# Kernel tuning notes

Hardware: AMD Instinct MI355X
Metric: run time of the kernel (lower is better)

Reference implementation:

```python
import jax, jax.numpy as jnp
import numpy as np
import math

NUM_HEADS = 12


def setup_inputs() -> dict:
    key = jax.random.key(0)
    ks = jax.random.split(key, 8)
    B, H, W, C = 8, 32, 32, 768
    dh = C // NUM_HEADS
    s = 0.02
    return {
        "x": jax.random.normal(ks[0], (B, H, W, C), dtype=jnp.float32),
        "w_qkv": jax.random.normal(ks[1], (C, 3 * C), dtype=jnp.float32) * s,
        "b_qkv": jnp.zeros((3 * C,), dtype=jnp.float32),
        "w_out": jax.random.normal(ks[2], (C, C), dtype=jnp.float32) * s,
        "b_out": jnp.zeros((C,), dtype=jnp.float32),
        "rel_pos_h": jax.random.normal(ks[3], (2 * H - 1, dh), dtype=jnp.float32) * s,
        "rel_pos_w": jax.random.normal(ks[4], (2 * W - 1, dh), dtype=jnp.float32) * s,
    }


def reference(x, w_qkv, b_qkv, w_out, b_out, rel_pos_h, rel_pos_w):
    B, H, W, C = x.shape
    nh = NUM_HEADS
    dh = C // nh
    scale = math.sqrt(dh)

    # QKV projection: (B, H*W, 3C) -> (3, B*nh, H*W, dh)
    qkv = jnp.einsum("bhwc,cf->bhwf", x, w_qkv) + b_qkv
    qkv = qkv.reshape(B, H * W, 3, nh, dh).transpose(2, 0, 3, 1, 4)
    qkv = qkv.reshape(3, B * nh, H * W, dh)
    q, k, v = qkv[0], qkv[1], qkv[2]

    scores = jnp.einsum("bqd,bkd->bqk", q, k) / scale  # (B*nh, HW, HW)

    # Decomposed relative position bias (q_size == k_size == input_size,
    # so get_rel_pos is a pure gather, no interpolation).
    coords_h = jnp.arange(H)[:, None] - jnp.arange(H)[None, :] + (H - 1)
    coords_w = jnp.arange(W)[:, None] - jnp.arange(W)[None, :] + (W - 1)
    Rh = rel_pos_h[coords_h]  # (H, H, dh)
    Rw = rel_pos_w[coords_w]  # (W, W, dh)
    r_q = q.reshape(B * nh, H, W, dh)
    rel_h = jnp.einsum("bhwc,hkc->bhwk", r_q, Rh)  # (B*nh, H, W, H)
    rel_w = jnp.einsum("bhwc,wkc->bhwk", r_q, Rw)  # (B*nh, H, W, W)
    scores = (
        scores.reshape(B * nh, H, W, H, W)
        + rel_h[:, :, :, :, None]
        + rel_w[:, :, :, None, :]
    ).reshape(B * nh, H * W, H * W)

    weights = jax.nn.softmax(scores, axis=-1)
    out = jnp.einsum("bqk,bkd->bqd", weights, v)  # (B*nh, HW, dh)
    out = out.reshape(B, nh, H, W, dh).transpose(0, 2, 3, 1, 4).reshape(B, H, W, C)
    return jnp.einsum("bhwc,cf->bhwf", out, w_out) + b_out
```

## Files before the change

### kernel.cpp

```cpp
#include <hip/hip_runtime.h>
#include <stdint.h>

#define NH 12
#define DH 64
#define HW_ 32
#define SEQ 1024
#define CDIM 768
#define BATCH 8
#define BHN (BATCH*NH)

#define LOG2E 1.44269504f
#define KSCALE 0.18033688f

typedef unsigned short u16;
typedef __attribute__((ext_vector_type(4))) float f32x4;
typedef __attribute__((ext_vector_type(8))) short bf16x8;

static __device__ __forceinline__ u16 f2bf(float f) {
  union { float f; unsigned u; } v; v.f = f;
  unsigned r = v.u + 0x7fff + ((v.u >> 16) & 1);
  return (u16)(r >> 16);
}
static __device__ __forceinline__ float bf2f(u16 h) {
  union { unsigned u; float f; } v; v.u = ((unsigned)h) << 16;
  return v.f;
}
static __device__ __forceinline__ unsigned pk_bf2(float a, float b) {
  union { float f; unsigned u; } ua, ub; ua.f = a; ub.f = b;
  return __builtin_amdgcn_perm(ub.u + 0x8000u, ua.u + 0x8000u, 0x07060302u);
}

#define GLDS(gp, lp) __builtin_amdgcn_global_load_lds( \
  (const __attribute__((address_space(1))) unsigned int*)(gp), \
  (__attribute__((address_space(3))) unsigned int*)(lp), 16, 0, 0)

__device__ __forceinline__ void transcvt_body(const float* __restrict__ w, u16* __restrict__ wt,
                                              int R, int C, int bx, int by, int tid) {
  __shared__ float t[64][65];
  const int tx = tid & 63, ty = tid >> 6;
  int c0 = bx * 64, r0 = by * 64;
  #pragma unroll
  for (int i = 0; i < 16; ++i) {
    int r = ty + i * 4;
    t[r][tx] = w[(size_t)(r0 + r) * C + c0 + tx];
  }
  __syncthreads();
  #pragma unroll
  for (int i = 0; i < 16; ++i) {
    int c = ty + i * 4;
    wt[(size_t)(c0 + c) * R + r0 + tx] = f2bf(t[tx][c]);
  }
}

__global__ void k_prep(const float* __restrict__ x, u16* __restrict__ xb,
                       const float* __restrict__ wqkv, u16* __restrict__ wqkvt,
                       const float* __restrict__ wout, u16* __restrict__ woutt) {
  const int bid = blockIdx.x, tid = threadIdx.x;
  if (bid < 6144) {
    int i = bid * 256 + tid;
    const float4 v = *(const float4*)(x + (size_t)i * 4);
    uint2 o;
    o.x = (unsigned)f2bf(v.x) | ((unsigned)f2bf(v.y) << 16);
    o.y = (unsigned)f2bf(v.z) | ((unsigned)f2bf(v.w) << 16);
    *(uint2*)(xb + (size_t)i * 4) = o;
  } else if (bid < 6144 + 432) {
    int b = bid - 6144;
    transcvt_body(wqkv, wqkvt, 768, 2304, b % 36, b / 36, tid);
  } else {
    int b = bid - 6144 - 432;
    transcvt_body(wout, woutt, 768, 768, b % 12, b / 12, tid);
  }
}

__global__ __launch_bounds__(256) void k_relbias2(
    const u16* __restrict__ Q, const float* __restrict__ rph,
    const float* __restrict__ rpw,
    float* __restrict__ bH, float* __restrict__ bW) {
  __shared__ float Gs[4][64][66];
  const int bh = blockIdx.y;
  const int tid = threadIdx.x, w = tid >> 6, l = tid & 63;
  const int rr = l & 15, g4 = l >> 4;
  const int p0 = blockIdx.x * 256 + w * 64;
  const u16* Qb = Q + ((size_t)bh * SEQ + p0) * DH;

  bf16x8 qa[4][2];
  #pragma unroll
  for (int rt = 0; rt < 4; ++rt)
    #pragma unroll
    for (int kk = 0; kk < 2; ++kk)
      qa[rt][kk] = *(const bf16x8*)&Qb[(size_t)(rt * 16 + rr) * DH + kk * 32 + g4 * 8];

  const int hq0 = p0 >> 5;
  #pragma unroll
  for (int g = 0; g < 2; ++g) {
    int hq = hq0 + g;
    #pragma unroll
    for (int ct = 0; ct < 2; ++ct) {
      bf16x8 bfr[2];
      #pragma unroll
      for (int kk = 0; kk < 2; ++kk) {
        const float* src = &rph[(size_t)(hq - (ct * 16 + rr) + 31) * DH + kk * 32 + g4 * 8];
        #pragma unroll
        for (int e = 0; e < 8; ++e) bfr[kk][e] = (short)f2bf(src[e]);
      }
      #pragma unroll
      for (int mt = 0; mt < 2; ++mt) {
        f32x4 acc = {};
        #pragma unroll
        for (int kk = 0; kk < 2; ++kk)
          acc = __builtin_amdgcn_mfma_f32_16x16x32_bf16(qa[g * 2 + mt][kk], bfr[kk], acc, 0, 0, 0);
        #pragma unroll
        for (int j = 0; j < 4; ++j) {
          int row = p0 + g * 32 + mt * 16 + g4 * 4 + j;
          bH[((size_t)bh * SEQ + row) * 32 + ct * 16 + rr] = acc[j] * LOG2E;
        }
      }
    }
  }

  #pragma unroll
  for (int jt = 0; jt < 4; ++jt) {
    int j_ = jt * 16 + rr; if (j_ > 62) j_ = 62;
    bf16x8 bfr[2];
    #pragma unroll
    for (int kk = 0; kk < 2; ++kk) {
      const float* src = &rpw[(size_t)j_ * DH + kk * 32 + g4 * 8];
      #pragma unroll
      for (int e = 0; e < 8; ++e) bfr[kk][e] = (short)f2bf(src[e]);
    }
    #pragma unroll
    for (int rt = 0; rt < 4; ++rt) {
      f32x4 acc = {};
      #pragma unroll
      for (int kk = 0; kk < 2; ++kk)
        acc = __builtin_amdgcn_mfma_f32_16x16x32_bf16(qa[rt][kk], bfr[kk], acc, 0, 0, 0);
      #pragma unroll
      for (int j = 0; j < 4; ++j)
        Gs[w][rt * 16 + g4 * 4 + j][jt * 16 + rr] = acc[j] * LOG2E;
    }
  }
  __syncthreads();
  #pragma unroll
  for (int wk = 0; wk < 32; ++wk)
    bW[((size_t)bh * SEQ + p0 + l) * 32 + wk] = Gs[w][l][(l & 31) - wk + 31];
}

template<int EPI, int NT>
__global__ __launch_bounds__(256) void k_gemm(
    const u16* __restrict__ A, const u16* __restrict__ Bt,
    const float* __restrict__ bias,
    void* __restrict__ o0, void* __restrict__ o1, void* __restrict__ o2,
    int nwg) {
  __shared__ u16 As[2][128][32];
  __shared__ u16 Bs[2][128][32];
  const int cpx = nwg >> 3;
  const int swz = (blockIdx.x & 7) * cpx + (blockIdx.x >> 3);
  const int tid = threadIdx.x, w = tid >> 6, l = tid & 63;
  const int wr = w >> 1, wc = w & 1;
  const int rr = l & 15, g4 = l >> 4;
  const int m0 = (swz / NT) * 128, n0 = (swz % NT) * 128;
  const int K = CDIM;
  f32x4 acc[4][4] = {};

  auto stage = [&](int buf, int t) {
    int k0 = t * 32;
    #pragma unroll
    for (int i = 0; i < 2; ++i) {
      int c = tid + i * 256;
      int row = c >> 2, kc = (c & 3) * 8;
      GLDS(A + (size_t)(m0 + row) * K + k0 + kc, ((u16*)As) + buf * 4096 + c * 8);
      GLDS(Bt + (size_t)(n0 + row) * K + k0 + kc, ((u16*)Bs) + buf * 4096 + c * 8);
    }
  };
  stage(0, 0);
  __syncthreads();
  for (int t = 0; t < K / 32; ++t) {
    const int cur = t & 1;
    if (t + 1 < K / 32) stage(cur ^ 1, t + 1);
    bf16x8 af[4], bfr[4];
    #pragma unroll
    for (int mm = 0; mm < 4; ++mm)
      af[mm] = *(const bf16x8*)(((const u16*)As) + cur * 4096 + (wr * 64 + mm * 16 + rr) * 32 + g4 * 8);
    #pragma unroll
    for (int nn = 0; nn < 4; ++nn)
      bfr[nn] = *(const bf16x8*)(((const u16*)Bs) + cur * 4096 + (wc * 64 + nn * 16 + rr) * 32 + g4 * 8);
    __builtin_amdgcn_s_setprio(1);
    #pragma unroll
    for (int mm = 0; mm < 4; ++mm)
      #pragma unroll
      for (int nn = 0; nn < 4; ++nn)
        acc[mm][nn] = __builtin_amdgcn_mfma_f32_16x16x32_bf16(af[mm], bfr[nn], acc[mm][nn], 0, 0, 0);
    __builtin_amdgcn_s_setprio(0);
    __syncthreads();
  }
  #pragma unroll
  for (int mm = 0; mm < 4; ++mm)
    #pragma unroll
    for (int nn = 0; nn < 4; ++nn) {
      int row0 = m0 + wr * 64 + mm * 16 + g4 * 4;
      int col = n0 + wc * 64 + nn * 16 + rr;
      float bb = bias[col];
      if (EPI == 0) {
        int which = col / CDIM, rem = col % CDIM;
        int hh = rem >> 6, d = rem & 63;
        int b = row0 >> 10, p = row0 & 1023;
        if (which == 2) {
          uint2 pk;
          pk.x = (unsigned)f2bf(acc[mm][nn][0] + bb) | ((unsigned)f2bf(acc[mm][nn][1] + bb) << 16);
          pk.y = (unsigned)f2bf(acc[mm][nn][2] + bb) | ((unsigned)f2bf(acc[mm][nn][3] + bb) << 16);
          *(uint2*)&((u16*)o2)[((size_t)(b * NH + hh) * DH + d) * SEQ + p] = pk;
        } else if (which == 1) {
          #pragma unroll
          for (int j = 0; j < 4; ++j)
            ((u16*)o1)[(((size_t)(b * NH + hh)) * SEQ + p + j) * DH + d] = f2bf((acc[mm][nn][j] + bb) * KSCALE);
        } else {
          #pragma unroll
          for (int j = 0; j < 4; ++j)
            ((u16*)o0)[(((size_t)(b * NH + hh)) * SEQ + p + j) * DH + d] = f2bf(acc[mm][nn][j] + bb);
        }
      } else {
        #pragma unroll
        for (int j = 0; j < 4; ++j)
          ((float*)o0)[(size_t)(row0 + j) * CDIM + col] = acc[mm][nn][j] + bb;
      }
    }
}

__global__ __launch_bounds__(512, 4) void k_attn(
    const u16* __restrict__ Q, const u16* __restrict__ Kg,
    const u16* __restrict__ Vtg,
    const float* __restrict__ bHg, const float* __restrict__ bWg,
    u16* __restrict__ O) {
  __shared__ u16 Ks[2][64][64];
  __shared__ u16 Vs[2][64][64];
  __shared__ u16 Ps[8][16][72];
  const int bid = blockIdx.x;
  const int bhi = bid % 96;
  const int q0 = (bid / 96) * 128;
  const int tid = threadIdx.x, w = tid >> 6, l = tid & 63;
  const int rr = l & 15, g4 = l >> 4;
  const u16* Qb = Q + (size_t)bhi * SEQ * DH;
  const u16* Kb = Kg + (size_t)bhi * SEQ * DH;
  const u16* Vb = Vtg + (size_t)bhi * SEQ * DH;

  bf16x8 qf[2];
  #pragma unroll
  for (int kk = 0; kk < 2; ++kk)
    qf[kk] = *(const bf16x8*)&Qb[(size_t)(q0 + w * 16 + rr) * DH + kk * 32 + g4 * 8];

  float4 bwv[4];
  float bh0[4], bh1[4];
  float lsum[4] = {};
  f32x4 oacc[4] = {};
  #pragma unroll
  for (int j = 0; j < 4; ++j) {
    int p_e = q0 + w * 16 + g4 * 4 + j;
    const float* bHrow = &bHg[((size_t)bhi * SEQ + p_e) * 32];
    const float* bWrow = &bWg[((size_t)bhi * SEQ + p_e) * 32];
    bwv[j] = *(const float4*)&bWrow[(4 * rr) & 31];
    bh0[j] = bHrow[rr];
    bh1[j] = bHrow[16 + rr];
  }

  auto stageKV = [&](int buf, int t) {
    int k0 = t * 64;
    int c = tid;
    int row = c >> 3, ci = c & 7;
    int swk = ci ^ ((row >> 2) & 7);
    int swv = ci ^ (row & 7);
    GLDS(Kb + (size_t)(k0 + row) * DH + swk * 8, ((u16*)Ks) + buf * 4096 + c * 8);
    GLDS(Vb + (size_t)row * SEQ + k0 + swv * 8, ((u16*)Vs) + buf * 4096 + c * 8);
  };
  stageKV(0, 0);
  __syncthreads();

  for (int t = 0; t < 16; ++t) {
    const int cur = t & 1;
    if (t + 1 < 16) stageKV(cur ^ 1, t + 1);

    bf16x8 kf[4][2];
    #pragma unroll
    for (int nn = 0; nn < 4; ++nn)
      #pragma unroll
      for (int kk = 0; kk < 2; ++kk) {
        int row = 4 * rr + nn;
        int ch = (kk * 4 + g4) ^ ((row >> 2) & 7);
        kf[nn][kk] = *(const bf16x8*)(((const u16*)Ks) + cur * 4096 + row * 64 + ch * 8);
      }
    f32x4 sc[4] = {};
    __builtin_amdgcn_s_setprio(1);
    #pragma unroll
    for (int nn = 0; nn < 4; ++nn)
      #pragma unroll
      for (int kk = 0; kk < 2; ++kk)
        sc[nn] = __builtin_amdgcn_mfma_f32_16x16x32_bf16(qf[kk], kf[nn][kk], sc[nn], 0, 0, 0);
    __builtin_amdgcn_s_setprio(0);

    int srcl = (l & 48) | ((2 * t + (rr >> 3)) & 15);
    #pragma unroll
    for (int j = 0; j < 4; ++j) {
      float bhsel = (t < 8) ? bh0[j] : bh1[j];
      float bh = __shfl(bhsel, srcl);
      float v0 = __builtin_amdgcn_exp2f(sc[0][j] + (bh + bwv[j].x));
      float v1 = __builtin_amdgcn_exp2f(sc[1][j] + (bh + bwv[j].y));
      float v2 = __builtin_amdgcn_exp2f(sc[2][j] + (bh + bwv[j].z));
      float v3 = __builtin_amdgcn_exp2f(sc[3][j] + (bh + bwv[j].w));
      lsum[j] += (v0 + v1) + (v2 + v3);
      uint2 pk;
      pk.x = pk_bf2(v0, v1);
      pk.y = pk_bf2(v2, v3);
      *(uint2*)&Ps[w][g4 * 4 + j][4 * rr] = pk;
    }

    bf16x8 pa[2], vf[4][2];
    #pragma unroll
    for (int kk = 0; kk < 2; ++kk)
      pa[kk] = *(const bf16x8*)&Ps[w][rr][kk * 32 + g4 * 8];
    #pragma unroll
    for (int nn = 0; nn < 4; ++nn)
      #pragma unroll
      for (int kk = 0; kk < 2; ++kk) {
        int row = nn * 16 + rr;
        int ch = (kk * 4 + g4) ^ (row & 7);
        vf[nn][kk] = *(const bf16x8*)(((const u16*)Vs) + cur * 4096 + row * 64 + ch * 8);
      }
    __builtin_amdgcn_s_setprio(1);
    #pragma unroll
    for (int nn = 0; nn < 4; ++nn)
      #pragma unroll
      for (int kk = 0; kk < 2; ++kk)
        oacc[nn] = __builtin_amdgcn_mfma_f32_16x16x32_bf16(pa[kk], vf[nn][kk], oacc[nn], 0, 0, 0);
    __builtin_amdgcn_s_setprio(0);
    __syncthreads();
  }

  const int b = bhi / NH, h = bhi % NH;
  #pragma unroll
  for (int j = 0; j < 4; ++j) {
    float lv = lsum[j];
    #pragma unroll
    for (int off = 1; off < 16; off <<= 1) lv += __shfl_xor(lv, off);
    float inv = 1.0f / lv;
    int p = q0 + w * 16 + g4 * 4 + j;
    #pragma unroll
    for (int nn = 0; nn < 4; ++nn) {
      int d = nn * 16 + rr;
      O[((size_t)(b * SEQ + p)) * CDIM + h * DH + d] = f2bf(oacc[nn][j] * inv);
    }
  }
}

extern "C" void kernel_launch(void* const* d_in, const int* in_sizes, int n_in,
                              void* d_out, int out_size, void* d_ws, size_t ws_size,
                              hipStream_t stream) {
  const float* x     = (const float*)d_in[0];
  const float* w_qkv = (const float*)d_in[1];
  const float* b_qkv = (const float*)d_in[2];
  const float* w_out = (const float*)d_in[3];
  const float* b_out = (const float*)d_in[4];
  const float* rph   = (const float*)d_in[5];
  const float* rpw   = (const float*)d_in[6];
  float* out = (float*)d_out;
  char* ws = (char*)d_ws;

  const size_t SZ = (size_t)BHN * SEQ * DH * 2;
  u16* Xb    = (u16*)(ws);
  u16* Wqkvt = (u16*)(ws + SZ);
  u16* Woutt = (u16*)(ws + SZ + 3538944);
  u16* Qd    = (u16*)(ws + SZ + 4718592);
  u16* Kd    = (u16*)(ws + 2 * SZ + 4718592);
  u16* Vd    = (u16*)(ws + 3 * SZ + 4718592);
  u16* Vt    = (u16*)(ws + 4 * SZ + 4718592);
  float* bW  = (float*)(ws + 5 * SZ + 4718592);
  float* bH  = (float*)Vd;
  u16* Ob    = Xb;
  if (ws_size < 6 * SZ + 4718592) return;

  k_prep<<<6720, 256, 0, stream>>>(x, Xb, w_qkv, Wqkvt, w_out, Woutt);
  k_gemm<0, 18><<<1152, 256, 0, stream>>>(Xb, Wqkvt, b_qkv, Qd, Kd, Vt, 1152);
  k_relbias2<<<dim3(4, 96), 256, 0, stream>>>(Qd, rph, rpw, bH, bW);
  k_attn<<<768, 512, 0, stream>>>(Qd, Kd, Vt, bH, bW, Ob);
  k_gemm<1, 6><<<384, 256, 0, stream>>>(Ob, Woutt, b_out, out, nullptr, nullptr, 384);
}
```

Baseline: 152.7 us.

## Fuse relative position bias computation into attention kernel prologue

Removes the separate k_relbias2 kernel and computes the height and width relative-position bias terms inside k_attn from the Q fragments already in registers, using MFMA against bf16-converted rel_pos tables. The width bias is staged through the K shared buffer before the main loop, with two extra barriers. This drops one launch and the global write and read of the bH and bW buffers, and shrinks the workspace. In exchange, each attention block now does the bias MFMAs and reads rph/rpw with scalar float loads in its prologue.

```diff
diff --git a/kernel.cpp b/kernel.cpp
--- a/kernel.cpp
+++ b/kernel.cpp
@@ -20,10 +20,6 @@
   union { float f; unsigned u; } v; v.f = f;
   unsigned r = v.u + 0x7fff + ((v.u >> 16) & 1);
   return (u16)(r >> 16);
-}
-static __device__ __forceinline__ float bf2f(u16 h) {
-  union { unsigned u; float f; } v; v.u = ((unsigned)h) << 16;
-  return v.f;
 }
 static __device__ __forceinline__ unsigned pk_bf2(float a, float b) {
   union { float f; unsigned u; } ua, ub; ua.f = a; ub.f = b;
@@ -70,79 +66,6 @@
     int b = bid - 6144 - 432;
     transcvt_body(wout, woutt, 768, 768, b % 12, b / 12, tid);
   }
-}
-
-__global__ __launch_bounds__(256) void k_relbias2(
-    const u16* __restrict__ Q, const float* __restrict__ rph,
-    const float* __restrict__ rpw,
-    float* __restrict__ bH, float* __restrict__ bW) {
-  __shared__ float Gs[4][64][66];
-  const int bh = blockIdx.y;
-  const int tid = threadIdx.x, w = tid >> 6, l = tid & 63;
-  const int rr = l & 15, g4 = l >> 4;
-  const int p0 = blockIdx.x * 256 + w * 64;
-  const u16* Qb = Q + ((size_t)bh * SEQ + p0) * DH;
-
-  bf16x8 qa[4][2];
-  #pragma unroll
-  for (int rt = 0; rt < 4; ++rt)
-    #pragma unroll
-    for (int kk = 0; kk < 2; ++kk)
-      qa[rt][kk] = *(const bf16x8*)&Qb[(size_t)(rt * 16 + rr) * DH + kk * 32 + g4 * 8];
-
-  const int hq0 = p0 >> 5;
-  #pragma unroll
-  for (int g = 0; g < 2; ++g) {
-    int hq = hq0 + g;
-    #pragma unroll
-    for (int ct = 0; ct < 2; ++ct) {
-      bf16x8 bfr[2];
-      #pragma unroll
-      for (int kk = 0; kk < 2; ++kk) {
-        const float* src = &rph[(size_t)(hq - (ct * 16 + rr) + 31) * DH + kk * 32 + g4 * 8];
-        #pragma unroll
-        for (int e = 0; e < 8; ++e) bfr[kk][e] = (short)f2bf(src[e]);
-      }
-      #pragma unroll
-      for (int mt = 0; mt < 2; ++mt) {
-        f32x4 acc = {};
-        #pragma unroll
-        for (int kk = 0; kk < 2; ++kk)
-          acc = __builtin_amdgcn_mfma_f32_16x16x32_bf16(qa[g * 2 + mt][kk], bfr[kk], acc, 0, 0, 0);
-        #pragma unroll
-        for (int j = 0; j < 4; ++j) {
-          int row = p0 + g * 32 + mt * 16 + g4 * 4 + j;
-          bH[((size_t)bh * SEQ + row) * 32 + ct * 16 + rr] = acc[j] * LOG2E;
-        }
-      }
-    }
-  }
-
-  #pragma unroll
-  for (int jt = 0; jt < 4; ++jt) {
-    int j_ = jt * 16 + rr; if (j_ > 62) j_ = 62;
-    bf16x8 bfr[2];
-    #pragma unroll
-    for (int kk = 0; kk < 2; ++kk) {
-      const float* src = &rpw[(size_t)j_ * DH + kk * 32 + g4 * 8];
-      #pragma unroll
-      for (int e = 0; e < 8; ++e) bfr[kk][e] = (short)f2bf(src[e]);
-    }
-    #pragma unroll
-    for (int rt = 0; rt < 4; ++rt) {
-      f32x4 acc = {};
-      #pragma unroll
-      for (int kk = 0; kk < 2; ++kk)
-        acc = __builtin_amdgcn_mfma_f32_16x16x32_bf16(qa[rt][kk], bfr[kk], acc, 0, 0, 0);
-      #pragma unroll
-      for (int j = 0; j < 4; ++j)
-        Gs[w][rt * 16 + g4 * 4 + j][jt * 16 + rr] = acc[j] * LOG2E;
-    }
-  }
-  __syncthreads();
-  #pragma unroll
-  for (int wk = 0; wk < 32; ++wk)
-    bW[((size_t)bh * SEQ + p0 + l) * 32 + wk] = Gs[w][l][(l & 31) - wk + 31];
 }
 
 template<int EPI, int NT>
@@ -229,7 +152,7 @@
 __global__ __launch_bounds__(512, 4) void k_attn(
     const u16* __restrict__ Q, const u16* __restrict__ Kg,
     const u16* __restrict__ Vtg,
-    const float* __restrict__ bHg, const float* __restrict__ bWg,
+    const float* __restrict__ rph, const float* __restrict__ rpw,
     u16* __restrict__ O) {
   __shared__ u16 Ks[2][64][64];
   __shared__ u16 Vs[2][64][64];
@@ -248,19 +171,58 @@
   for (int kk = 0; kk < 2; ++kk)
     qf[kk] = *(const bf16x8*)&Qb[(size_t)(q0 + w * 16 + rr) * DH + kk * 32 + g4 * 8];
 
+  const int hq = (q0 >> 5) + (w >> 1);
+  float bh0[4], bh1[4];
+  {
+    f32x4 accH[2] = {{}, {}};
+    #pragma unroll
+    for (int nn = 0; nn < 2; ++nn) {
+      bf16x8 bfr[2];
+      #pragma unroll
+      for (int kk = 0; kk < 2; ++kk) {
+        const float* src = &rph[(size_t)(hq - (nn * 16 + rr) + 31) * DH + kk * 32 + g4 * 8];
+        #pragma unroll
+        for (int e = 0; e < 8; ++e) bfr[kk][e] = (short)f2bf(src[e]);
+      }
+      #pragma unroll
+      for (int kk = 0; kk < 2; ++kk)
+        accH[nn] = __builtin_amdgcn_mfma_f32_16x16x32_bf16(qf[kk], bfr[kk], accH[nn], 0, 0, 0);
+    }
+    #pragma unroll
+    for (int j = 0; j < 4; ++j) { bh0[j] = accH[0][j] * LOG2E; bh1[j] = accH[1][j] * LOG2E; }
+  }
+
+  float* Gf = (float*)&Ks[0][0][0];
+  #pragma unroll
+  for (int nn = 0; nn < 4; ++nn) {
+    int j_ = nn * 16 + rr; if (j_ > 62) j_ = 62;
+    bf16x8 bfr[2];
+    #pragma unroll
+    for (int kk = 0; kk < 2; ++kk) {
+      const float* src = &rpw[(size_t)j_ * DH + kk * 32 + g4 * 8];
+      #pragma unroll
+      for (int e = 0; e < 8; ++e) bfr[kk][e] = (short)f2bf(src[e]);
+    }
+    f32x4 acc = {};
+    #pragma unroll
+    for (int kk = 0; kk < 2; ++kk)
+      acc = __builtin_amdgcn_mfma_f32_16x16x32_bf16(qf[kk], bfr[kk], acc, 0, 0, 0);
+    #pragma unroll
+    for (int j = 0; j < 4; ++j)
+      Gf[w * 1024 + (g4 * 4 + j) * 64 + nn * 16 + rr] = acc[j] * LOG2E;
+  }
+  __syncthreads();
   float4 bwv[4];
-  float bh0[4], bh1[4];
+  #pragma unroll
+  for (int j = 0; j < 4; ++j) {
+    int c0 = ((q0 + w * 16 + g4 * 4 + j) & 31) + 31 - 4 * (rr & 7);
+    const float* gr = &Gf[w * 1024 + (g4 * 4 + j) * 64];
+    bwv[j].x = gr[c0]; bwv[j].y = gr[c0 - 1]; bwv[j].z = gr[c0 - 2]; bwv[j].w = gr[c0 - 3];
+  }
+  __syncthreads();
+
   float lsum[4] = {};
   f32x4 oacc[4] = {};
-  #pragma unroll
-  for (int j = 0; j < 4; ++j) {
-    int p_e = q0 + w * 16 + g4 * 4 + j;
-    const float* bHrow = &bHg[((size_t)bhi * SEQ + p_e) * 32];
-    const float* bWrow = &bWg[((size_t)bhi * SEQ + p_e) * 32];
-    bwv[j] = *(const float4*)&bWrow[(4 * rr) & 31];
-    bh0[j] = bHrow[rr];
-    bh1[j] = bHrow[16 + rr];
-  }
 
   auto stageKV = [&](int buf, int t) {
     int k0 = t * 64;
@@ -369,16 +331,12 @@
   u16* Woutt = (u16*)(ws + SZ + 3538944);
   u16* Qd    = (u16*)(ws + SZ + 4718592);
   u16* Kd    = (u16*)(ws + 2 * SZ + 4718592);
-  u16* Vd    = (u16*)(ws + 3 * SZ + 4718592);
-  u16* Vt    = (u16*)(ws + 4 * SZ + 4718592);
-  float* bW  = (float*)(ws + 5 * SZ + 4718592);
-  float* bH  = (float*)Vd;
+  u16* Vt    = (u16*)(ws + 3 * SZ + 4718592);
   u16* Ob    = Xb;
-  if (ws_size < 6 * SZ + 4718592) return;
+  if (ws_size < 4 * SZ + 4718592) return;
 
   k_prep<<<6720, 256, 0, stream>>>(x, Xb, w_qkv, Wqkvt, w_out, Woutt);
   k_gemm<0, 18><<<1152, 256, 0, stream>>>(Xb, Wqkvt, b_qkv, Qd, Kd, Vt, 1152);
-  k_relbias2<<<dim3(4, 96), 256, 0, stream>>>(Qd, rph, rpw, bH, bW);
-  k_attn<<<768, 512, 0, stream>>>(Qd, Kd, Vt, bH, bW, Ob);
+  k_attn<<<768, 512, 0, stream>>>(Qd, Kd, Vt, rph, rpw, Ob);
   k_gemm<1, 6><<<384, 256, 0, stream>>>(Ob, Woutt, b_out, out, nullptr, nullptr, 384);
 }
```

After: 148.0 us. -3.0%, faster.
